# Optimization experiments

Hardware: AMD Instinct MI355X
Metric: run time of the kernel (lower is better)

The kernel has to match this reference:

```python
import jax, jax.numpy as jnp
import numpy as np

# Hyper-params from init_kwargs
H, DM, DA, DP, M, T = 8, 512, 256, 128, 32, 4096
DK, DAh, DPh = DM // H, DA // H, DP // H   # 64, 32, 16
B, K_STEPS = 8, 2048
S = T + K_STEPS          # length of x = memory + x_pre
EPS = 1e-12

def _l2n(x):
    # F.normalize(p=2, dim=-1)
    return x / jnp.maximum(jnp.linalg.norm(x, axis=-1, keepdims=True), EPS)

def setup_inputs() -> dict:
    key = jax.random.key(0)
    ks = jax.random.split(key, 28)
    n = lambda i, s, sc=0.05: jax.random.normal(ks[i], s, jnp.float32) * sc
    return {
        "memory": jax.random.normal(ks[0], (B, S - 1, DM), jnp.float32),
        "x_pre":  jax.random.normal(ks[1], (B, 1, DM), jnp.float32),
        "aux":    jax.random.normal(ks[2], (B, S, DA), jnp.float32),
        "pos":    jax.random.normal(ks[3], (B, S, DP), jnp.float32),
        "Wq": n(4, (H, DK, DM)), "bq": n(5, (H, DK)),
        "Wk": n(6, (H, DK, DM)), "bk": n(7, (H, DK)),
        "Wv": n(8, (H, DK, DM)), "bv": n(9, (H, DK)),
        "Wqa": n(10, (H, DAh, DA)), "bqa": n(11, (H, DAh)),
        "Wka": n(12, (H, DAh, DA)), "bka": n(13, (H, DAh)),
        "Wqp": n(14, (H, DPh, DP)), "bqp": n(15, (H, DPh)),
        "Wkp": n(16, (H, DPh, DP)), "bkp": n(17, (H, DPh)),
        "W_ih": n(18, (3 * DK, DM)), "W_hh": n(19, (3 * DK, DK)),
        "b_ih": n(20, (3 * DK,)), "b_hh": n(21, (3 * DK,)),
        "WO": n(22, (DM, DM)), "bO": n(23, (DM,)),
        "w": n(24, (1, 1), 1.0), "w_a": n(25, (1, 1), 1.0), "w_p": n(26, (1, 1), 1.0),
        "G": (jax.random.uniform(ks[27], (DK, DK)) < 0.5).astype(jnp.int32),
        "k": K_STEPS,
    }

def _forward(memory, x_pre, aux, pos, Wq, bq, Wk, bk, Wv, bv, Wqa, bqa, Wka, bka,
             Wqp, bqp, Wkp, bkp, W_ih, W_hh, b_ih, b_hh, WO, bO, w, w_a, w_p, G, k):
    b = memory.shape[0]
    x = jnp.concatenate([memory, x_pre], axis=1)           # [B, S, DM]
    s = x.shape[1]
    Wn = k + T - M + 1                                     # attention window length
    g = G.astype(x.dtype)
    mask_h = jnp.tile(g, (1, H))[None]                     # [1, DK, DM] per-head SparseLinear mask

    # per-head Q/K node projections (SparseLinear), L2-normalized
    Q = _l2n(jnp.einsum('bsd,hkd->bhsk', x, Wq * mask_h) + bq[None, :, None, :])
    K = _l2n(jnp.einsum('bsd,hkd->bhsk', x, Wk * mask_h) + bk[None, :, None, :])

    # tn_transform_pre: for each position p, mean over the M-step window of Qv[m].K[p+m]
    Qv = Q[:, :, -M:, :]                                   # [B,H,M,DK]
    D = jnp.einsum('bhmd,bhsd->bhms', Qv, K)               # [B,H,M,S]
    p_idx = jnp.arange(Wn)[None, :] + jnp.arange(M)[:, None]   # [M,Wn]
    band = D[:, :, jnp.arange(M)[:, None], p_idx]          # [B,H,M,Wn] band-diagonal gather
    tn = band.mean(axis=2)                                 # [B,H,Wn]

    # aux / pos similarities: only the last query row survives the slice in the source
    QA = _l2n(jnp.einsum('bsa,hca->bhsc', aux, Wqa) + bqa[None, :, None, :])
    KA = _l2n(jnp.einsum('bsa,hca->bhsc', aux, Wka) + bka[None, :, None, :])
    dot2 = jnp.einsum('bhc,bhsc->bhs', QA[:, :, -1, :], KA[:, :, aux.shape[1] - Wn:, :])
    QP = _l2n(jnp.einsum('bsp,hcp->bhsc', pos, Wqp) + bqp[None, :, None, :])
    KP = _l2n(jnp.einsum('bsp,hcp->bhsc', pos, Wkp) + bkp[None, :, None, :])
    dot3 = jnp.einsum('bhc,bhsc->bhs', QP[:, :, -1, :], KP[:, :, pos.shape[1] - Wn:, :])

    attn = jax.nn.softmax(w[0, 0] * tn + w_a[0, 0] * dot2 + w_p[0, 0] * dot3, axis=-1)  # [B,H,Wn]

    # value projection over the history window, weighted by attn[..., :-1]
    xv = x[:, s - Wn:s - 1, :]                             # [B, Wn-1, DM]
    V = jnp.einsum('bsd,hkd->bhsk', xv, Wv * mask_h) + bv[None, :, None, :]
    hist = jnp.einsum('bhw,bhwd->bhd', attn[:, :, :-1], V) # [B,H,DK]

    # sequential GRU over the recent M-1 steps (shared across heads)
    recent = jnp.swapaxes(x[:, -M:-1, :], 0, 1)            # [M-1, B, DM]
    def cell(hprev, xt):
        gi = xt @ W_ih.T + b_ih
        gh = hprev @ W_hh.T + b_hh
        ir, iz, inn = jnp.split(gi, 3, axis=-1)
        hr, hz, hn = jnp.split(gh, 3, axis=-1)
        r = jax.nn.sigmoid(ir + hr)
        z = jax.nn.sigmoid(iz + hz)
        nst = jnp.tanh(inn + r * hn)
        return (1.0 - z) * nst + z * hprev, None
    res, _ = jax.lax.scan(cell, jnp.zeros((b, DK), x.dtype), recent)  # [B, DK]

    # concat per-head deltas (deta[:, :, 1:] just drops the initial zeros column)
    deta = (hist + attn[:, :, -1:] * res[:, None, :]).reshape(b, H * DK)   # [B, DM]
    mask_o = jnp.tile(g, (H, H))                           # [DM, DM] for W_O
    out = x_pre + (deta @ (WO * mask_o).T + bO)[:, None, :]
    return out

def reference(memory, x_pre, aux, pos, Wq, bq, Wk, bk, Wv, bv, Wqa, bqa, Wka, bka,
              Wqp, bqp, Wkp, bkp, W_ih, W_hh, b_ih, b_hh, WO, bO, w, w_a, w_p, G, k):
    return _forward(memory, x_pre, aux, pos, Wq, bq, Wk, bk, Wv, bv, Wqa, bqa, Wka,
                    bka, Wqp, bqp, Wkp, bkp, W_ih, W_hh, b_ih, b_hh, WO, bO,
                    w, w_a, w_p, G, k)
```

## Files before the change

### kernel.cpp

```cpp
#include <hip/hip_runtime.h>
#include <math.h>

#define BB   8
#define S    6144
#define SM1  6143
#define DM   512
#define H    8
#define DK   64
#define M    32
#define WN   6113
#define DA   256
#define DAh  32
#define DP   128
#define DPh  16
#define EPSN 1e-12f

#define WS_WKT    0
#define WS_WKAT   262144
#define WS_WKPT   327680
#define WS_QHAT   344064
#define WS_QAHAT  475136
#define WS_QPHAT  477184
#define WS_LOGITS 478208
#define WS_XBAR   869440
#define WS_ALAST  902208
#define WS_RES    902272
#define WS_GI     902784
#define WS_WQM    950400
#define WS_XBF    1212544
#define N_LOGITS  391232
#define N_XBAR    32768

typedef __attribute__((ext_vector_type(8))) short short8;
typedef __attribute__((ext_vector_type(4))) float f32x4;

__device__ inline unsigned short f2bf(float f) {
    union { float f; unsigned u; } v; v.f = f;
    unsigned r = v.u + 0x7fffu + ((v.u >> 16) & 1u);
    return (unsigned short)(r >> 16);
}
__device__ inline float bf2f(unsigned short u) {
    union { unsigned u; float f; } v; v.u = ((unsigned)u) << 16; return v.f;
}

union S8U { short8 v; unsigned short e[8]; };

#define PREP_NB 2368
#define GI_NB   248
#define XCAST_NB 12288

__global__ __launch_bounds__(256) void prelude_k(
    const float* __restrict__ Wk, const float* __restrict__ Wka,
    const float* __restrict__ Wkp, const float* __restrict__ Wq,
    const int* __restrict__ G,
    unsigned short* __restrict__ wkb, unsigned short* __restrict__ wkab,
    unsigned short* __restrict__ wkpb, float* __restrict__ wqm,
    const float* __restrict__ memory, const float* __restrict__ x_pre,
    const float* __restrict__ W_ih, const float* __restrict__ b_ih,
    float* __restrict__ gi_all, unsigned short* __restrict__ xbf)
{
    int bx = blockIdx.x, tid = threadIdx.x;

    if (bx < PREP_NB) {
        int idx = bx * 256 + tid;
        if (idx < H*DM*DK) {
            int k = idx & 63; int d = (idx >> 6) & 511; int h = idx >> 15;
            float v = Wk[(size_t)(h*DK + k)*DM + d] * (float)G[k*DK + (d & 63)];
            wkb[(size_t)h*DM*DK + (((d >> 3)*DK + k) << 3) + (d & 7)] = f2bf(v);
        }
        int i2 = idx - H*DM*DK;
        if (i2 >= 0 && i2 < H*DA*DAh) {
            int h = i2 >> 13; int r = i2 & 8191;
            int j = r & 7; int f = r >> 3;
            int c = f & 31; int a = (f >> 5)*8 + j;
            wkab[i2] = f2bf(Wka[(size_t)(h*DAh + c)*DA + a]);
        }
        int i3 = idx - H*DM*DK - H*DA*DAh;
        if (i3 >= 0 && i3 < H*DP*DPh) {
            int h = i3 >> 11; int r = i3 & 2047;
            int j = r & 7; int f = r >> 3;
            int c = f & 15; int p = (f >> 4)*8 + j;
            wkpb[i3] = f2bf(Wkp[(size_t)(h*DPh + c)*DP + p]);
        }
        int i4 = idx - H*DM*DK - H*DA*DAh - H*DP*DPh;
        if (i4 >= 0 && i4 < H*DK*DM) {
            int d = i4 & 511; int k = (i4 >> 9) & 63;
            wqm[i4] = Wq[i4] * (float)G[k*DK + (d & 63)];
        }
        return;
    }
    if (bx < PREP_NB + GI_NB) {
        if (tid < 192) {
            int gx = bx - PREP_NB;
            int t = gx >> 3, b = gx & 7, c = tid;
            const float* xr = memory + ((size_t)b*SM1 + (S - M) + t)*DM;
            const float* wr = W_ih + (size_t)c*DM;
            float s = b_ih[c];
            for (int d = 0; d < DM; d += 4) {
                float4 x4 = *(const float4*)(xr + d);
                float4 w4 = *(const float4*)(wr + d);
                s += x4.x*w4.x + x4.y*w4.y + x4.z*w4.z + x4.w*w4.w;
            }
            gi_all[((size_t)t*BB + b)*192 + c] = s;
        }
        return;
    }
    {
        size_t e = ((size_t)(bx - PREP_NB - GI_NB)*256 + tid)*8;
        int b = (int)(e / ((size_t)S*DM));
        size_t r = e - (size_t)b*S*DM;
        int t = (int)(r >> 9);
        int d = (int)(r & 511);
        const float* src = (t < SM1) ? memory + ((size_t)b*SM1 + t)*DM + d
                                     : x_pre + (size_t)b*DM + d;
        float4 v0 = *(const float4*)src, v1 = *(const float4*)(src + 4);
        S8U t8;
        t8.e[0]=f2bf(v0.x); t8.e[1]=f2bf(v0.y); t8.e[2]=f2bf(v0.z); t8.e[3]=f2bf(v0.w);
        t8.e[4]=f2bf(v1.x); t8.e[5]=f2bf(v1.y); t8.e[6]=f2bf(v1.z); t8.e[7]=f2bf(v1.w);
        *(short8*)(xbf + e) = t8.v;
    }
}

__global__ __launch_bounds__(256) void qhat_k2(
    const float* __restrict__ memory, const float* __restrict__ x_pre,
    const float* __restrict__ wqm, const float* __restrict__ bq,
    float* __restrict__ qhat)
{
    int bx = blockIdx.x;
    int mp = bx & 15;
    int h  = (bx >> 4) & 7;
    int b  = bx >> 7;
    int tid = threadIdx.x;
    int k = tid & 63, dq = tid >> 6;

    int m0 = mp*2;
    int t0 = S - M + m0, t1 = t0 + 1;
    const float* x0 = ((t0 < SM1) ? memory + ((size_t)b*SM1 + t0)*DM
                                  : x_pre + (size_t)b*DM) + dq*128;
    const float* x1 = ((t1 < SM1) ? memory + ((size_t)b*SM1 + t1)*DM
                                  : x_pre + (size_t)b*DM) + dq*128;
    const float* wr = wqm + (size_t)(h*DK + k)*DM + dq*128;

    float s0 = 0.f, s1 = 0.f;
    #pragma unroll 8
    for (int d = 0; d < 128; d += 4) {
        float4 w4 = *(const float4*)(wr + d);
        float4 a4 = *(const float4*)(x0 + d);
        float4 b4 = *(const float4*)(x1 + d);
        s0 += w4.x*a4.x + w4.y*a4.y + w4.z*a4.z + w4.w*a4.w;
        s1 += w4.x*b4.x + w4.y*b4.y + w4.z*b4.z + w4.w*b4.w;
    }

    __shared__ float part[2][4][64];
    part[0][dq][k] = s0;
    part[1][dq][k] = s1;
    __syncthreads();

    if (tid < 128) {
        int mi = tid >> 6;
        int kk = tid & 63;
        float q = part[mi][0][kk] + part[mi][1][kk] + part[mi][2][kk] + part[mi][3][kk]
                + bq[h*DK + kk];
        float ss = q*q;
        #pragma unroll
        for (int d2 = 1; d2 <= 32; d2 <<= 1) ss += __shfl_xor(ss, d2);
        qhat[((size_t)(b*H + h)*M + (m0 + mi))*DK + kk] = q / fmaxf(sqrtf(ss), EPSN);
    }
}

__global__ __launch_bounds__(256) void qaqp_k(
    const float* __restrict__ aux, const float* __restrict__ pos,
    const float* __restrict__ Wqa, const float* __restrict__ bqa,
    const float* __restrict__ Wqp, const float* __restrict__ bqp,
    float* __restrict__ qahat, float* __restrict__ qphat)
{
    int bh = blockIdx.x; int b = bh >> 3, h = bh & 7;
    int tid = threadIdx.x;
    __shared__ float pa[32][8];
    __shared__ float pp[16][16];

    {
        int c = tid & 31, ch = tid >> 5;
        const float* ar = aux + ((size_t)b*S + (S-1))*DA + ch*32;
        const float* wv = Wqa + (size_t)(h*DAh + c)*DA + ch*32;
        float s = 0.f;
        #pragma unroll
        for (int a = 0; a < 32; a += 4) {
            float4 a4 = *(const float4*)(ar + a);
            float4 w4 = *(const float4*)(wv + a);
            s += a4.x*w4.x + a4.y*w4.y + a4.z*w4.z + a4.w*w4.w;
        }
        pa[c][ch] = s;
    }
    {
        int c = tid & 15, ch = tid >> 4;
        const float* pr = pos + ((size_t)b*S + (S-1))*DP + ch*8;
        const float* wv = Wqp + (size_t)(h*DPh + c)*DP + ch*8;
        float4 a4 = *(const float4*)(pr);
        float4 w4 = *(const float4*)(wv);
        float4 a5 = *(const float4*)(pr + 4);
        float4 w5 = *(const float4*)(wv + 4);
        pp[c][ch] = a4.x*w4.x + a4.y*w4.y + a4.z*w4.z + a4.w*w4.w
                  + a5.x*w5.x + a5.y*w5.y + a5.z*w5.z + a5.w*w5.w;
    }
    __syncthreads();

    if (tid < 32) {
        float q = bqa[h*DAh + tid];
        #pragma unroll
        for (int ch = 0; ch < 8; ++ch) q += pa[tid][ch];
        float ss = q*q;
        #pragma unroll
        for (int d2 = 1; d2 <= 16; d2 <<= 1) ss += __shfl_xor(ss, d2);
        qahat[(size_t)bh*DAh + tid] = q / fmaxf(sqrtf(ss), EPSN);
    } else if (tid >= 64 && tid < 80) {
        int c = tid - 64;
        float q = bqp[h*DPh + c];
        #pragma unroll
        for (int ch = 0; ch < 16; ++ch) q += pp[c][ch];
        float ss = q*q;
        #pragma unroll
        for (int d2 = 1; d2 <= 8; d2 <<= 1) ss += __shfl_xor(ss, d2);
        qphat[(size_t)bh*DPh + c] = q / fmaxf(sqrtf(ss), EPSN);
    }
}

#define SMEM_BYTES 33280

__device__ __forceinline__ void kproj3_body(int bxx, int tid, unsigned char* smemraw,
    const unsigned short* __restrict__ xbf, const unsigned short* __restrict__ wkb,
    const float* __restrict__ bk, const float* __restrict__ qhat,
    const float* __restrict__ wscal, float* __restrict__ logits)
{
    int tile = bxx % 96, h = (bxx / 96) & 7, b = bxx / (96*8);
    int t0 = tile * 64;
    int wave = tid >> 6, lane = tid & 63;
    int quad = lane >> 4, l16 = lane & 15;

    typedef unsigned short row72[72];
    row72* Qs = (row72*)smemraw;
    row72* Kb = (row72*)(smemraw + 32*72*2);
    float* tnloc = (float*)(smemraw + 96*72*2);

    {
        const float* qsrc = qhat + (size_t)(b*H + h)*M*DK;
        int i = tid * 8;
        float4 a0 = *(const float4*)(qsrc + i);
        float4 a1 = *(const float4*)(qsrc + i + 4);
        S8U t8;
        t8.e[0]=f2bf(a0.x); t8.e[1]=f2bf(a0.y); t8.e[2]=f2bf(a0.z); t8.e[3]=f2bf(a0.w);
        t8.e[4]=f2bf(a1.x); t8.e[5]=f2bf(a1.y); t8.e[6]=f2bf(a1.z); t8.e[7]=f2bf(a1.w);
        *(short8*)&Qs[i >> 6][i & 63] = t8.v;
    }
    if (tid < 95) tnloc[tid] = 0.f;

    f32x4 acc[4];
    #pragma unroll
    for (int nt = 0; nt < 4; ++nt) acc[nt] = (f32x4){0.f,0.f,0.f,0.f};

    const unsigned short* xrow = xbf + ((size_t)b*S + t0 + wave*16 + l16)*DM;
    const unsigned short* wh = wkb + (size_t)h*DM*DK;

    #pragma unroll
    for (int ch = 0; ch < 4; ++ch) {
        #pragma unroll
        for (int ks = 0; ks < 4; ++ks) {
            short8 a = *(const short8*)(xrow + ch*128 + ks*32 + quad*8);
            #pragma unroll
            for (int nt = 0; nt < 4; ++nt) {
                short8 bf = *(const short8*)(wh + (((ch*16 + ks*4 + quad)*DK) + nt*16 + l16)*8);
                acc[nt] = __builtin_amdgcn_mfma_f32_16x16x32_bf16(a, bf, acc[nt], 0, 0, 0);
            }
        }
    }

    {
        float vv[4][4];
        float ss[4] = {0.f, 0.f, 0.f, 0.f};
        #pragma unroll
        for (int nt = 0; nt < 4; ++nt) {
            float bkv = bk[h*DK + nt*16 + l16];
            #pragma unroll
            for (int reg = 0; reg < 4; ++reg) {
                float v = acc[nt][reg] + bkv;
                vv[nt][reg] = v;
                ss[reg] += v*v;
            }
        }
        #pragma unroll
        for (int d2 = 1; d2 <= 8; d2 <<= 1)
            #pragma unroll
            for (int reg = 0; reg < 4; ++reg) ss[reg] += __shfl_xor(ss[reg], d2);
        #pragma unroll
        for (int reg = 0; reg < 4; ++reg) {
            float inv = 1.f / fmaxf(sqrtf(ss[reg]), EPSN);
            #pragma unroll
            for (int nt = 0; nt < 4; ++nt)
                Kb[wave*16 + quad*4 + reg][nt*16 + l16] = f2bf(vv[nt][reg] * inv);
        }
    }
    __syncthreads();

    {
        int mtile = wave & 1;
        int thalf = (wave >> 1) * 32;
        f32x4 acc2[2];
        acc2[0] = (f32x4){0.f,0.f,0.f,0.f};
        acc2[1] = (f32x4){0.f,0.f,0.f,0.f};
        #pragma unroll
        for (int ks = 0; ks < 2; ++ks) {
            short8 a = *(const short8*)&Qs[mtile*16 + l16][ks*32 + quad*8];
            #pragma unroll
            for (int nt = 0; nt < 2; ++nt) {
                short8 kf = *(const short8*)&Kb[thalf + nt*16 + l16][ks*32 + quad*8];
                acc2[nt] = __builtin_amdgcn_mfma_f32_16x16x32_bf16(a, kf, acc2[nt], 0, 0, 0);
            }
        }
        int m0 = mtile*16 + quad*4;
        #pragma unroll
        for (int nt = 0; nt < 2; ++nt) {
            int tl = thalf + nt*16 + l16;
            #pragma unroll
            for (int reg = 0; reg < 4; ++reg) {
                int mm = m0 + reg;
                int j = t0 + tl - mm;
                if (j >= 0 && j < WN)
                    atomicAdd(&tnloc[tl - mm + 31], acc2[nt][reg]);
            }
        }
    }
    __syncthreads();
    if (tid < 95) {
        int j = t0 + tid - 31;
        if (j >= 0 && j < WN)
            atomicAdd(&logits[(size_t)(b*H + h)*WN + j], wscal[0]*(1.f/32.f)*tnloc[tid]);
    }
}

__device__ __forceinline__ void ka_body(int g, int tid, unsigned char* smemraw,
    const float* __restrict__ aux, const unsigned short* __restrict__ wkab,
    const float* __restrict__ bka, const float* __restrict__ qahat,
    const float* __restrict__ wa, float* __restrict__ logits)
{
    int tile = g % 96;
    int b    = g / 96;
    int j0   = tile * 64;
    int wave = tid >> 6, lane = tid & 63;
    int quad = lane >> 4, l16 = lane & 15;

    unsigned short* Xa = (unsigned short*)smemraw;

    {
        int r = tid >> 2, seg = tid & 3;
        int j = j0 + r; if (j > WN-1) j = WN-1;
        const float* ar = aux + ((size_t)b*S + (31 + j))*DA + seg*64;
        int tt = r >> 4, lo = r & 15;
        #pragma unroll
        for (int gg = 0; gg < 8; ++gg) {
            float4 v0 = *(const float4*)(ar + gg*8);
            float4 v1 = *(const float4*)(ar + gg*8 + 4);
            int d0 = seg*64 + gg*8;
            int ks = d0 >> 5, qd = (d0 >> 3) & 3;
            S8U t8;
            t8.e[0]=f2bf(v0.x); t8.e[1]=f2bf(v0.y); t8.e[2]=f2bf(v0.z); t8.e[3]=f2bf(v0.w);
            t8.e[4]=f2bf(v1.x); t8.e[5]=f2bf(v1.y); t8.e[6]=f2bf(v1.z); t8.e[7]=f2bf(v1.w);
            *(short8*)&Xa[(tt*8 + ks)*520 + (qd*16 + lo)*8] = t8.v;
        }
    }
    __syncthreads();

    float wav = wa[0];
    for (int h = 0; h < H; ++h) {
        const unsigned short* wsrc = wkab + (size_t)h*DA*DAh;
        f32x4 acc[2];
        acc[0] = (f32x4){0.f,0.f,0.f,0.f};
        acc[1] = (f32x4){0.f,0.f,0.f,0.f};
        #pragma unroll
        for (int ks = 0; ks < 8; ++ks) {
            short8 a = *(const short8*)&Xa[(wave*8 + ks)*520 + lane*8];
            #pragma unroll
            for (int nt = 0; nt < 2; ++nt) {
                short8 bf = *(const short8*)(wsrc + (size_t)(((ks*4 + quad)*32) + nt*16 + l16)*8);
                acc[nt] = __builtin_amdgcn_mfma_f32_16x16x32_bf16(a, bf, acc[nt], 0, 0, 0);
            }
        }
        float bk0 = bka[h*DAh + l16], bk1 = bka[h*DAh + 16 + l16];
        float q0 = qahat[(size_t)(b*H + h)*DAh + l16];
        float q1 = qahat[(size_t)(b*H + h)*DAh + 16 + l16];
        #pragma unroll
        for (int reg = 0; reg < 4; ++reg) {
            float v0 = acc[0][reg] + bk0;
            float v1 = acc[1][reg] + bk1;
            float ss = v0*v0 + v1*v1;
            float dp = v0*q0 + v1*q1;
            #pragma unroll
            for (int d2 = 1; d2 <= 8; d2 <<= 1) {
                ss += __shfl_xor(ss, d2);
                dp += __shfl_xor(dp, d2);
            }
            if (l16 == 0) {
                int j = j0 + wave*16 + quad*4 + reg;
                if (j < WN)
                    atomicAdd(&logits[(size_t)(b*H + h)*WN + j],
                              wav * dp / fmaxf(sqrtf(ss), EPSN));
            }
        }
    }
}

__device__ __forceinline__ void kp_body(int g, int tid, unsigned char* smemraw,
    const float* __restrict__ pos, const unsigned short* __restrict__ wkpb,
    const float* __restrict__ bkp, const float* __restrict__ qphat,
    const float* __restrict__ wp, float* __restrict__ logits)
{
    int tile = g % 96;
    int b    = g / 96;
    int j0   = tile * 64;
    int wave = tid >> 6, lane = tid & 63;
    int quad = lane >> 4, l16 = lane & 15;

    unsigned short* Xp = (unsigned short*)smemraw;

    {
        int r = tid >> 2, seg = tid & 3;
        int j = j0 + r; if (j > WN-1) j = WN-1;
        const float* pr = pos + ((size_t)b*S + (31 + j))*DP + seg*32;
        int tt = r >> 4, lo = r & 15;
        #pragma unroll
        for (int gg = 0; gg < 4; ++gg) {
            float4 v0 = *(const float4*)(pr + gg*8);
            float4 v1 = *(const float4*)(pr + gg*8 + 4);
            int d0 = seg*32 + gg*8;
            int ks = d0 >> 5, qd = (d0 >> 3) & 3;
            S8U t8;
            t8.e[0]=f2bf(v0.x); t8.e[1]=f2bf(v0.y); t8.e[2]=f2bf(v0.z); t8.e[3]=f2bf(v0.w);
            t8.e[4]=f2bf(v1.x); t8.e[5]=f2bf(v1.y); t8.e[6]=f2bf(v1.z); t8.e[7]=f2bf(v1.w);
            *(short8*)&Xp[(tt*4 + ks)*520 + (qd*16 + lo)*8] = t8.v;
        }
    }
    __syncthreads();

    float wpv = wp[0];
    for (int h = 0; h < H; ++h) {
        const unsigned short* wsrc = wkpb + (size_t)h*DP*DPh;
        f32x4 acc = (f32x4){0.f,0.f,0.f,0.f};
        #pragma unroll
        for (int ks = 0; ks < 4; ++ks) {
            short8 a = *(const short8*)&Xp[(wave*4 + ks)*520 + lane*8];
            short8 bf = *(const short8*)(wsrc + (size_t)(((ks*4 + quad)*16) + l16)*8);
            acc = __builtin_amdgcn_mfma_f32_16x16x32_bf16(a, bf, acc, 0, 0, 0);
        }
        float bk0 = bkp[h*DPh + l16];
        float q0 = qphat[(size_t)(b*H + h)*DPh + l16];
        #pragma unroll
        for (int reg = 0; reg < 4; ++reg) {
            float v = acc[reg] + bk0;
            float ss = v*v;
            float dp = v*q0;
            #pragma unroll
            for (int d2 = 1; d2 <= 8; d2 <<= 1) {
                ss += __shfl_xor(ss, d2);
                dp += __shfl_xor(dp, d2);
            }
            if (l16 == 0) {
                int j = j0 + wave*16 + quad*4 + reg;
                if (j < WN)
                    atomicAdd(&logits[(size_t)(b*H + h)*WN + j],
                              wpv * dp / fmaxf(sqrtf(ss), EPSN));
            }
        }
    }
}

__global__ __launch_bounds__(256, 4) void proj_fused_k(
    const unsigned short* __restrict__ xbf, const unsigned short* __restrict__ wkb,
    const float* __restrict__ bk, const float* __restrict__ qhat,
    const float* __restrict__ w,
    const float* __restrict__ aux, const unsigned short* __restrict__ wkab,
    const float* __restrict__ bka, const float* __restrict__ qahat,
    const float* __restrict__ wa,
    const float* __restrict__ pos, const unsigned short* __restrict__ wkpb,
    const float* __restrict__ bkp, const float* __restrict__ qphat,
    const float* __restrict__ wp,
    float* __restrict__ logits)
{
    __shared__ __align__(16) unsigned char smemraw[SMEM_BYTES];
    int bx = blockIdx.x;
    int g = bx / 10, r = bx - g*10;
    int tid = threadIdx.x;
    if (r < 8)
        kproj3_body(g*8 + r, tid, smemraw, xbf, wkb, bk, qhat, w, logits);
    else if (r == 8)
        ka_body(g, tid, smemraw, aux, wkab, bka, qahat, wa, logits);
    else
        kp_body(g, tid, smemraw, pos, wkpb, bkp, qphat, wp, logits);
}

__global__ __launch_bounds__(256, 2) void ka_only_k(
    const float* __restrict__ aux, const unsigned short* __restrict__ wkab,
    const float* __restrict__ bka, const float* __restrict__ qahat,
    const float* __restrict__ wa, float* __restrict__ logits)
{
    __shared__ __align__(16) unsigned char smemraw[SMEM_BYTES];
    ka_body(blockIdx.x, threadIdx.x, smemraw, aux, wkab, bka, qahat, wa, logits);
}
__global__ __launch_bounds__(256, 2) void kp_only_k(
    const float* __restrict__ pos, const unsigned short* __restrict__ wkpb,
    const float* __restrict__ bkp, const float* __restrict__ qphat,
    const float* __restrict__ wp, float* __restrict__ logits)
{
    __shared__ __align__(16) unsigned char smemraw[SMEM_BYTES];
    kp_body(blockIdx.x, threadIdx.x, smemraw, pos, wkpb, bkp, qphat, wp, logits);
}

__global__ __launch_bounds__(256, 2) void kproj_band_mfma2(
    const float* __restrict__ memory, const float* __restrict__ x_pre,
    const unsigned short* __restrict__ wkb, const float* __restrict__ bk,
    const float* __restrict__ qhat, const float* __restrict__ wscal,
    float* __restrict__ logits)
{
    int bx = blockIdx.x;
    int hp = bx & 3, b = (bx >> 2) & 7, tile = bx >> 5;
    int t0 = tile * 128;
    int tid = threadIdx.x;
    int wave = tid >> 6, lane = tid & 63;
    int quad = lane >> 4, l16 = lane & 15;

    __shared__ unsigned short Xf[32*520];
    __shared__ unsigned short Wf[16*520];
    __shared__ unsigned short Kb[128][72];
    __shared__ unsigned short Qs[M][72];
    __shared__ float tnloc[159];

    if (tid < 159) tnloc[tid] = 0.f;
    {
        int h = hp*2;
        const float* qsrc = qhat + (size_t)(b*H + h)*M*DK;
        int i = tid * 8;
        float4 a0 = *(const float4*)(qsrc + i);
        float4 a1 = *(const float4*)(qsrc + i + 4);
        S8U t8;
        t8.e[0]=f2bf(a0.x); t8.e[1]=f2bf(a0.y); t8.e[2]=f2bf(a0.z); t8.e[3]=f2bf(a0.w);
        t8.e[4]=f2bf(a1.x); t8.e[5]=f2bf(a1.y); t8.e[6]=f2bf(a1.z); t8.e[7]=f2bf(a1.w);
        *(short8*)&Qs[i >> 6][i & 63] = t8.v;
    }

    f32x4 acc[2][2][4];
    #pragma unroll
    for (int hi = 0; hi < 2; ++hi)
        #pragma unroll
        for (int mt = 0; mt < 2; ++mt)
            #pragma unroll
            for (int nt = 0; nt < 4; ++nt) acc[hi][mt][nt] = (f32x4){0.f,0.f,0.f,0.f};

    for (int ch = 0; ch < 4; ++ch) {
        __syncthreads();
        {
            int r = tid >> 1, half = tid & 1;
            int t = t0 + r;
            const float* xr = ((t < SM1) ? (memory + ((size_t)b*SM1 + t)*DM)
                                         : (x_pre + (size_t)b*DM)) + ch*128 + half*64;
            int tt = r >> 4, lo = r & 15;
            #pragma unroll
            for (int g = 0; g < 8; ++g) {
                float4 v0 = *(const float4*)(xr + g*8);
                float4 v1 = *(const float4*)(xr + g*8 + 4);
                int d0 = half*64 + g*8;
                int ks = d0 >> 5, qd = (d0 >> 3) & 3;
                S8U t8;
                t8.e[0]=f2bf(v0.x); t8.e[1]=f2bf(v0.y); t8.e[2]=f2bf(v0.z); t8.e[3]=f2bf(v0.w);
                t8.e[4]=f2bf(v1.x); t8.e[5]=f2bf(v1.y); t8.e[6]=f2bf(v1.z); t8.e[7]=f2bf(v1.w);
                *(short8*)&Xf[(tt*4 + ks)*520 + (qd*16 + lo)*8] = t8.v;
            }
        }
        {
// ... 160 lines not shown
    }
    float inv = 1.f / red[0];
    for (int j = tid; j < WN; j += 1024) {
        float a = expf(L[j] - mx) * inv;
        L[j] = a;
        if (j == WN-1) alast[bh] = a;
    }
}

#define JC2 96
__global__ __launch_bounds__(256) void xbar_bf_k(
    const unsigned short* __restrict__ xbf, const float* __restrict__ attn,
    float* __restrict__ xbar)
{
    int chunk = blockIdx.x & 63;
    int b = blockIdx.x >> 6;
    int j0 = chunk * JC2;
    int lim = (WN-1) - j0; if (lim > JC2) lim = JC2; if (lim < 0) lim = 0;
    __shared__ float al[H][JC2];
    int tid = threadIdx.x;
    for (int i = tid; i < H*JC2; i += 256) {
        int hh = i / JC2, jj = i - hh*JC2;
        al[hh][jj] = (jj < lim) ? attn[(size_t)(b*H + hh)*WN + j0 + jj] : 0.f;
    }
    __syncthreads();
    int d0 = tid * 2;
    const unsigned* p = (const unsigned*)(xbf + ((size_t)b*S + 31 + j0)*DM + d0);
    float acc[H][2];
    #pragma unroll
    for (int hh = 0; hh < H; ++hh) { acc[hh][0] = 0.f; acc[hh][1] = 0.f; }
    #pragma unroll 4
    for (int jj = 0; jj < lim; ++jj) {
        unsigned u = p[(size_t)jj*(DM/2)];
        float x0 = bf2f((unsigned short)(u & 0xffff));
        float x1 = bf2f((unsigned short)(u >> 16));
        #pragma unroll
        for (int hh = 0; hh < H; ++hh) {
            float a = al[hh][jj];
            acc[hh][0] += a * x0;
            acc[hh][1] += a * x1;
        }
    }
    #pragma unroll
    for (int hh = 0; hh < H; ++hh) {
        atomicAdd(&xbar[(size_t)(b*H+hh)*DM + d0],     acc[hh][0]);
        atomicAdd(&xbar[(size_t)(b*H+hh)*DM + d0 + 1], acc[hh][1]);
    }
}

#define JC 191
__global__ __launch_bounds__(256) void xbar_k(
    const float* __restrict__ memory, const float* __restrict__ attn,
    float* __restrict__ xbar)
{
    int chunk = blockIdx.x & 31;
    int b = blockIdx.x >> 5;
    int j0 = chunk * JC;
    __shared__ float al[H][JC];
    int tid = threadIdx.x;
    for (int i = tid; i < H*JC; i += 256) {
        int hh = i / JC, jj = i - hh*JC;
        al[hh][jj] = attn[(size_t)(b*H + hh)*WN + j0 + jj];
    }
    __syncthreads();
    int d0 = tid * 2;
    float acc[H][2];
    #pragma unroll
    for (int hh = 0; hh < H; ++hh) { acc[hh][0] = 0.f; acc[hh][1] = 0.f; }
    for (int jj = 0; jj < JC; ++jj) {
        int t = 31 + j0 + jj;
        const float2 xv = *(const float2*)(memory + ((size_t)b*SM1 + t)*DM + d0);
        #pragma unroll
        for (int hh = 0; hh < H; ++hh) {
            float a = al[hh][jj];
            acc[hh][0] += a * xv.x;
            acc[hh][1] += a * xv.y;
        }
    }
    #pragma unroll
    for (int hh = 0; hh < H; ++hh) {
        atomicAdd(&xbar[(size_t)(b*H+hh)*DM + d0],     acc[hh][0]);
        atomicAdd(&xbar[(size_t)(b*H+hh)*DM + d0 + 1], acc[hh][1]);
    }
}

__global__ __launch_bounds__(512) void gru_scan(
    const float* __restrict__ gi_all, const float* __restrict__ W_hh,
    const float* __restrict__ b_hh, float* __restrict__ res)
{
    int b = threadIdx.x >> 6;
    int l = threadIdx.x & 63;

    float w0[64], w1[64], w2[64];
    {
        const float* r0p = W_hh + (size_t)l*DK;
        const float* r1p = W_hh + (size_t)(64 + l)*DK;
        const float* r2p = W_hh + (size_t)(128 + l)*DK;
        #pragma unroll
        for (int i = 0; i < 16; ++i) {
            float4 a = *(const float4*)(r0p + i*4);
            w0[i*4]=a.x; w0[i*4+1]=a.y; w0[i*4+2]=a.z; w0[i*4+3]=a.w;
            float4 c = *(const float4*)(r1p + i*4);
            w1[i*4]=c.x; w1[i*4+1]=c.y; w1[i*4+2]=c.z; w1[i*4+3]=c.w;
            float4 e = *(const float4*)(r2p + i*4);
            w2[i*4]=e.x; w2[i*4+1]=e.y; w2[i*4+2]=e.z; w2[i*4+3]=e.w;
        }
    }
    float bh0 = b_hh[l], bh1 = b_hh[64 + l], bh2 = b_hh[128 + l];

    float h = 0.f;
    const float* g0 = gi_all + (size_t)b*192;
    float gr = g0[l], gz = g0[64 + l], gn = g0[128 + l];

    #pragma unroll 1
    for (int t = 0; t < 31; ++t) {
        float a0 = bh0, a1 = bh1, a2 = bh2;
        #pragma unroll
        for (int k = 0; k < 64; ++k) {
            float hk = __int_as_float(__builtin_amdgcn_readlane(__float_as_int(h), k));
            a0 += hk * w0[k];
            a1 += hk * w1[k];
            a2 += hk * w2[k];
        }
        float ngr = 0.f, ngz = 0.f, ngn = 0.f;
        if (t < 30) {
            const float* g2 = gi_all + ((size_t)(t+1)*BB + b)*192;
            ngr = g2[l]; ngz = g2[64 + l]; ngn = g2[128 + l];
        }
        float r = 1.f / (1.f + expf(-(gr + a0)));
        float z = 1.f / (1.f + expf(-(gz + a1)));
        float n = tanhf(gn + r * a2);
        h = (1.f - z)*n + z*h;
        gr = ngr; gz = ngz; gn = ngn;
    }
    res[b*DK + l] = h;
}

__global__ __launch_bounds__(512) void final_k(
    const float* __restrict__ x_pre, const float* __restrict__ xbar,
    const float* __restrict__ Wv, const float* __restrict__ bv,
    const float* __restrict__ WO, const float* __restrict__ bO,
    const float* __restrict__ alast, const float* __restrict__ res,
    const int* __restrict__ G, float* __restrict__ out)
{
    int b = blockIdx.x;
    int tid = threadIdx.x;
    __shared__ float gl[64*64];
    __shared__ float deta[512];
    for (int i = tid; i < 4096; i += 512) gl[i] = (float)G[(i & 63)*64 + (i >> 6)];
    __syncthreads();
    int h = tid >> 6, dk = tid & 63;
    float ala = alast[b*H + h];
    const float* xb  = xbar + (size_t)(b*H + h)*DM;
    const float* wvr = Wv + (size_t)tid*DM;
    const float* gcol = gl + dk;
    float s = 0.f;
    for (int e = 0; e < DM; e += 4) {
        float4 wv4 = *(const float4*)(wvr + e);
        float4 xb4 = *(const float4*)(xb + e);
        int eb = e & 63;
        s += wv4.x*gcol[eb*64]     *xb4.x + wv4.y*gcol[(eb+1)*64]*xb4.y
           + wv4.z*gcol[(eb+2)*64]*xb4.z + wv4.w*gcol[(eb+3)*64]*xb4.w;
    }
    float hist = s + bv[tid]*(1.f - ala);
    deta[tid] = hist + ala * res[b*DK + dk];
    __syncthreads();
    int dpos = tid;
    const float* wor = WO + (size_t)dpos*DM;
    const float* gcol2 = gl + (dpos & 63);
    float o = 0.f;
    for (int jj = 0; jj < DM; jj += 4) {
        float4 wo4 = *(const float4*)(wor + jj);
        int jb = jj & 63;
        o += wo4.x*gcol2[jb*64]     *deta[jj]   + wo4.y*gcol2[(jb+1)*64]*deta[jj+1]
           + wo4.z*gcol2[(jb+2)*64]*deta[jj+2] + wo4.w*gcol2[(jb+3)*64]*deta[jj+3];
    }
    out[(size_t)b*DM + dpos] = x_pre[(size_t)b*DM + dpos] + o + bO[dpos];
}

extern "C" void kernel_launch(void* const* d_in, const int* in_sizes, int n_in,
                              void* d_out, int out_size, void* d_ws, size_t ws_size,
                              hipStream_t stream)
{
    const float* memory = (const float*)d_in[0];
    const float* x_pre  = (const float*)d_in[1];
    const float* aux    = (const float*)d_in[2];
    const float* pos    = (const float*)d_in[3];
    const float* Wq  = (const float*)d_in[4];
    const float* bq  = (const float*)d_in[5];
    const float* Wk  = (const float*)d_in[6];
    const float* bk  = (const float*)d_in[7];
    const float* Wv  = (const float*)d_in[8];
    const float* bv  = (const float*)d_in[9];
    const float* Wqa = (const float*)d_in[10];
    const float* bqa = (const float*)d_in[11];
    const float* Wka = (const float*)d_in[12];
    const float* bka = (const float*)d_in[13];
    const float* Wqp = (const float*)d_in[14];
    const float* bqp = (const float*)d_in[15];
    const float* Wkp = (const float*)d_in[16];
    const float* bkp = (const float*)d_in[17];
    const float* W_ih = (const float*)d_in[18];
    const float* W_hh = (const float*)d_in[19];
    const float* b_ih = (const float*)d_in[20];
    const float* b_hh = (const float*)d_in[21];
    const float* WO  = (const float*)d_in[22];
    const float* bO  = (const float*)d_in[23];
    const float* w   = (const float*)d_in[24];
    const float* w_a = (const float*)d_in[25];
    const float* w_p = (const float*)d_in[26];
    const int*   G   = (const int*)d_in[27];
    (void)in_sizes; (void)n_in; (void)out_size;

    float* ws = (float*)d_ws;
    unsigned short* wkb  = (unsigned short*)(ws + WS_WKT);
    unsigned short* wkab = (unsigned short*)(ws + WS_WKAT);
    unsigned short* wkpb = (unsigned short*)(ws + WS_WKPT);
    float* qhat   = ws + WS_QHAT;
    float* qahat  = ws + WS_QAHAT;
    float* qphat  = ws + WS_QPHAT;
    float* logits = ws + WS_LOGITS;
    float* xbar   = ws + WS_XBAR;
    float* alast  = ws + WS_ALAST;
    float* resb   = ws + WS_RES;
    float* gi_all = ws + WS_GI;
    float* wqm    = ws + WS_WQM;
    unsigned short* xbf = (unsigned short*)(ws + WS_XBF);
    float* outp   = (float*)d_out;

    const size_t need = ((size_t)WS_XBF + 12582912) * 4;
    const bool big = (ws_size >= need);

    hipMemsetAsync(logits, 0, (size_t)(N_LOGITS + N_XBAR)*sizeof(float), stream);

    prelude_k<<<big ? (PREP_NB + GI_NB + XCAST_NB) : (PREP_NB + GI_NB), 256, 0, stream>>>(
        Wk, Wka, Wkp, Wq, G, wkb, wkab, wkpb, wqm,
        memory, x_pre, W_ih, b_ih, gi_all, xbf);

    qhat_k2<<<BB*H*16, 256, 0, stream>>>(memory, x_pre, wqm, bq, qhat);
    qaqp_k<<<BB*H, 256, 0, stream>>>(aux, pos, Wqa, bqa, Wqp, bqp, qahat, qphat);
    gru_scan<<<1, 512, 0, stream>>>(gi_all, W_hh, b_hh, resb);

    if (big) {
        proj_fused_k<<<7680, 256, 0, stream>>>(
            xbf, wkb, bk, qhat, w,
            aux, wkab, bka, qahat, w_a,
            pos, wkpb, bkp, qphat, w_p, logits);
    } else {
        kproj_band_mfma2<<<48*BB*4, 256, 0, stream>>>(memory, x_pre, wkb, bk, qhat,
                                                      w, logits);
        ka_only_k<<<BB*96, 256, 0, stream>>>(aux, wkab, bka, qahat, w_a, logits);
        kp_only_k<<<BB*96, 256, 0, stream>>>(pos, wkpb, bkp, qphat, w_p, logits);
    }

    softmax_k<<<BB*H, 1024, 0, stream>>>(logits, alast);

    if (big)
        xbar_bf_k<<<BB*64, 256, 0, stream>>>(xbf, logits, xbar);
    else
        xbar_k<<<BB*32, 256, 0, stream>>>(memory, logits, xbar);

    final_k<<<BB, 512, 0, stream>>>(x_pre, xbar, Wv, bv, WO, bO, alast, resb, G, outp);
}
```

Before: 615.6 us.

## Fuse small launches, stage K-proj activations in LDS, and split aux/pos heads across blocks

Folds the qa/qp query projection into the prelude kernel and merges the qhat and GRU-scan kernels into one launch, so the GRU now runs as two blocks of four batches each. This cuts the number of kernel launches and lets the tiny serial GRU overlap with the qhat blocks. The K-projection body now stages each activation chunk in shared memory through a register prefetch pipeline instead of reading it straight from global memory. The aux/pos logit bodies are split so each block handles two heads instead of eight, and the fused projection grid is regrouped from 10 to 4 slots per group for more parallelism. The costs are extra barriers, more shared memory per block, and the aux/pos tiles being reloaded once per head pair.

```diff
diff --git a/kernel.cpp b/kernel.cpp
--- a/kernel.cpp
+++ b/kernel.cpp
@@ -45,8 +45,9 @@
 
 union S8U { short8 v; unsigned short e[8]; };
 
-#define PREP_NB 2368
-#define GI_NB   248
+#define PREP_NB  2368
+#define GI_NB    248
+#define QAQP_NB  64
 #define XCAST_NB 12288
 
 __global__ __launch_bounds__(256) void prelude_k(
@@ -57,9 +58,15 @@
     unsigned short* __restrict__ wkpb, float* __restrict__ wqm,
     const float* __restrict__ memory, const float* __restrict__ x_pre,
     const float* __restrict__ W_ih, const float* __restrict__ b_ih,
-    float* __restrict__ gi_all, unsigned short* __restrict__ xbf)
+    float* __restrict__ gi_all, unsigned short* __restrict__ xbf,
+    const float* __restrict__ aux, const float* __restrict__ pos,
+    const float* __restrict__ Wqa, const float* __restrict__ bqa,
+    const float* __restrict__ Wqp, const float* __restrict__ bqp,
+    float* __restrict__ qahat, float* __restrict__ qphat)
 {
     int bx = blockIdx.x, tid = threadIdx.x;
+    __shared__ float pa[32][8];
+    __shared__ float pp[16][16];
 
     if (bx < PREP_NB) {
         int idx = bx * 256 + tid;
@@ -105,8 +112,56 @@
         }
         return;
     }
+    if (bx < PREP_NB + GI_NB + QAQP_NB) {
+        int bh = bx - PREP_NB - GI_NB;
+        int b = bh >> 3, h = bh & 7;
+        {
+            int c = tid & 31, ch = tid >> 5;
+            const float* ar = aux + ((size_t)b*S + (S-1))*DA + ch*32;
+            const float* wv = Wqa + (size_t)(h*DAh + c)*DA + ch*32;
+            float s = 0.f;
+            #pragma unroll
+            for (int a = 0; a < 32; a += 4) {
+                float4 a4 = *(const float4*)(ar + a);
+                float4 w4 = *(const float4*)(wv + a);
+                s += a4.x*w4.x + a4.y*w4.y + a4.z*w4.z + a4.w*w4.w;
+            }
+            pa[c][ch] = s;
+        }
+        {
+            int c = tid & 15, ch = tid >> 4;
+            const float* pr = pos + ((size_t)b*S + (S-1))*DP + ch*8;
+            const float* wv = Wqp + (size_t)(h*DPh + c)*DP + ch*8;
+            float4 a4 = *(const float4*)(pr);
+            float4 w4 = *(const float4*)(wv);
+            float4 a5 = *(const float4*)(pr + 4);
+            float4 w5 = *(const float4*)(wv + 4);
+            pp[c][ch] = a4.x*w4.x + a4.y*w4.y + a4.z*w4.z + a4.w*w4.w
+                      + a5.x*w5.x + a5.y*w5.y + a5.z*w5.z + a5.w*w5.w;
+        }
+        __syncthreads();
+        if (tid < 32) {
+            float q = bqa[h*DAh + tid];
+            #pragma unroll
+            for (int ch = 0; ch < 8; ++ch) q += pa[tid][ch];
+            float ss = q*q;
+            #pragma unroll
+            for (int d2 = 1; d2 <= 16; d2 <<= 1) ss += __shfl_xor(ss, d2);
+            qahat[(size_t)bh*DAh + tid] = q / fmaxf(sqrtf(ss), EPSN);
+        } else if (tid >= 64 && tid < 80) {
+            int c = tid - 64;
+            float q = bqp[h*DPh + c];
+            #pragma unroll
+            for (int ch = 0; ch < 16; ++ch) q += pp[c][ch];
+            float ss = q*q;
+            #pragma unroll
+            for (int d2 = 1; d2 <= 8; d2 <<= 1) ss += __shfl_xor(ss, d2);
+            qphat[(size_t)bh*DPh + c] = q / fmaxf(sqrtf(ss), EPSN);
+        }
+        return;
+    }
     {
-        size_t e = ((size_t)(bx - PREP_NB - GI_NB)*256 + tid)*8;
+        size_t e = ((size_t)(bx - PREP_NB - GI_NB - QAQP_NB)*256 + tid)*8;
         int b = (int)(e / ((size_t)S*DM));
         size_t r = e - (size_t)b*S*DM;
         int t = (int)(r >> 9);
@@ -121,107 +176,106 @@
     }
 }
 
-__global__ __launch_bounds__(256) void qhat_k2(
+__global__ __launch_bounds__(256) void qhat_gru_k(
     const float* __restrict__ memory, const float* __restrict__ x_pre,
     const float* __restrict__ wqm, const float* __restrict__ bq,
-    float* __restrict__ qhat)
+    float* __restrict__ qhat,
+    const float* __restrict__ gi_all, const float* __restrict__ W_hh,
+    const float* __restrict__ b_hh, float* __restrict__ res)
 {
     int bx = blockIdx.x;
-    int mp = bx & 15;
-    int h  = (bx >> 4) & 7;
-    int b  = bx >> 7;
     int tid = threadIdx.x;
-    int k = tid & 63, dq = tid >> 6;
-
-    int m0 = mp*2;
-    int t0 = S - M + m0, t1 = t0 + 1;
-    const float* x0 = ((t0 < SM1) ? memory + ((size_t)b*SM1 + t0)*DM
-                                  : x_pre + (size_t)b*DM) + dq*128;
-    const float* x1 = ((t1 < SM1) ? memory + ((size_t)b*SM1 + t1)*DM
-                                  : x_pre + (size_t)b*DM) + dq*128;
-    const float* wr = wqm + (size_t)(h*DK + k)*DM + dq*128;
-
-    float s0 = 0.f, s1 = 0.f;
-    #pragma unroll 8
-    for (int d = 0; d < 128; d += 4) {
-        float4 w4 = *(const float4*)(wr + d);
-        float4 a4 = *(const float4*)(x0 + d);
-        float4 b4 = *(const float4*)(x1 + d);
-        s0 += w4.x*a4.x + w4.y*a4.y + w4.z*a4.z + w4.w*a4.w;
-        s1 += w4.x*b4.x + w4.y*b4.y + w4.z*b4.z + w4.w*b4.w;
-    }
-
     __shared__ float part[2][4][64];
-    part[0][dq][k] = s0;
-    part[1][dq][k] = s1;
-    __syncthreads();
-
-    if (tid < 128) {
-        int mi = tid >> 6;
-        int kk = tid & 63;
-        float q = part[mi][0][kk] + part[mi][1][kk] + part[mi][2][kk] + part[mi][3][kk]
-                + bq[h*DK + kk];
-        float ss = q*q;
-        #pragma unroll
-        for (int d2 = 1; d2 <= 32; d2 <<= 1) ss += __shfl_xor(ss, d2);
-        qhat[((size_t)(b*H + h)*M + (m0 + mi))*DK + kk] = q / fmaxf(sqrtf(ss), EPSN);
-    }
-}
-
-__global__ __launch_bounds__(256) void qaqp_k(
-    const float* __restrict__ aux, const float* __restrict__ pos,
-    const float* __restrict__ Wqa, const float* __restrict__ bqa,
-    const float* __restrict__ Wqp, const float* __restrict__ bqp,
-    float* __restrict__ qahat, float* __restrict__ qphat)
-{
-    int bh = blockIdx.x; int b = bh >> 3, h = bh & 7;
-    int tid = threadIdx.x;
-    __shared__ float pa[32][8];
-    __shared__ float pp[16][16];
+
+    if (bx < 1024) {
+        int mp = bx & 15;
+        int h  = (bx >> 4) & 7;
+        int b  = bx >> 7;
+        int k = tid & 63, dq = tid >> 6;
+
+        int m0 = mp*2;
+        int t0 = S - M + m0, t1 = t0 + 1;
+        const float* x0 = ((t0 < SM1) ? memory + ((size_t)b*SM1 + t0)*DM
+                                      : x_pre + (size_t)b*DM) + dq*128;
+        const float* x1 = ((t1 < SM1) ? memory + ((size_t)b*SM1 + t1)*DM
+                                      : x_pre + (size_t)b*DM) + dq*128;
+        const float* wr = wqm + (size_t)(h*DK + k)*DM + dq*128;
+
+        float s0 = 0.f, s1 = 0.f;
+        #pragma unroll 8
+        for (int d = 0; d < 128; d += 4) {
+            float4 w4 = *(const float4*)(wr + d);
+            float4 a4 = *(const float4*)(x0 + d);
+            float4 b4 = *(const float4*)(x1 + d);
+            s0 += w4.x*a4.x + w4.y*a4.y + w4.z*a4.z + w4.w*a4.w;
+            s1 += w4.x*b4.x + w4.y*b4.y + w4.z*b4.z + w4.w*b4.w;
+        }
+
+        part[0][dq][k] = s0;
+        part[1][dq][k] = s1;
+        __syncthreads();
+
+        if (tid < 128) {
+            int mi = tid >> 6;
+            int kk = tid & 63;
+            float q = part[mi][0][kk] + part[mi][1][kk] + part[mi][2][kk] + part[mi][3][kk]
+                    + bq[h*DK + kk];
+            float ss = q*q;
+            #pragma unroll
+            for (int d2 = 1; d2 <= 32; d2 <<= 1) ss += __shfl_xor(ss, d2);
+            qhat[((size_t)(b*H + h)*M + (m0 + mi))*DK + kk] = q / fmaxf(sqrtf(ss), EPSN);
+        }
+        return;
+    }
 
     {
-        int c = tid & 31, ch = tid >> 5;
-        const float* ar = aux + ((size_t)b*S + (S-1))*DA + ch*32;
-        const float* wv = Wqa + (size_t)(h*DAh + c)*DA + ch*32;
-        float s = 0.f;
-        #pragma unroll
-        for (int a = 0; a < 32; a += 4) {
-            float4 a4 = *(const float4*)(ar + a);
-            float4 w4 = *(const float4*)(wv + a);
-            s += a4.x*w4.x + a4.y*w4.y + a4.z*w4.z + a4.w*w4.w;
-        }
-        pa[c][ch] = s;
-    }
-    {
-        int c = tid & 15, ch = tid >> 4;
-        const float* pr = pos + ((size_t)b*S + (S-1))*DP + ch*8;
-        const float* wv = Wqp + (size_t)(h*DPh + c)*DP + ch*8;
-        float4 a4 = *(const float4*)(pr);
-        float4 w4 = *(const float4*)(wv);
-        float4 a5 = *(const float4*)(pr + 4);
-        float4 w5 = *(const float4*)(wv + 4);
-        pp[c][ch] = a4.x*w4.x + a4.y*w4.y + a4.z*w4.z + a4.w*w4.w
-                  + a5.x*w5.x + a5.y*w5.y + a5.z*w5.z + a5.w*w5.w;
-    }
-    __syncthreads();
-
-    if (tid < 32) {
-        float q = bqa[h*DAh + tid];
-        #pragma unroll
-        for (int ch = 0; ch < 8; ++ch) q += pa[tid][ch];
-        float ss = q*q;
-        #pragma unroll
-        for (int d2 = 1; d2 <= 16; d2 <<= 1) ss += __shfl_xor(ss, d2);
-        qahat[(size_t)bh*DAh + tid] = q / fmaxf(sqrtf(ss), EPSN);
-    } else if (tid >= 64 && tid < 80) {
-        int c = tid - 64;
-        float q = bqp[h*DPh + c];
-        #pragma unroll
-        for (int ch = 0; ch < 16; ++ch) q += pp[c][ch];
-        float ss = q*q;
-        #pragma unroll
-        for (int d2 = 1; d2 <= 8; d2 <<= 1) ss += __shfl_xor(ss, d2);
-        qphat[(size_t)bh*DPh + c] = q / fmaxf(sqrtf(ss), EPSN);
+        int bg = bx - 1024;
+        int b = bg*4 + (tid >> 6);
+        int l = tid & 63;
+
+        float w0[64], w1[64], w2[64];
+        {
+            const float* r0p = W_hh + (size_t)l*DK;
+            const float* r1p = W_hh + (size_t)(64 + l)*DK;
+            const float* r2p = W_hh + (size_t)(128 + l)*DK;
+            #pragma unroll
+            for (int i = 0; i < 16; ++i) {
+                float4 a = *(const float4*)(r0p + i*4);
+                w0[i*4]=a.x; w0[i*4+1]=a.y; w0[i*4+2]=a.z; w0[i*4+3]=a.w;
+                float4 c = *(const float4*)(r1p + i*4);
+                w1[i*4]=c.x; w1[i*4+1]=c.y; w1[i*4+2]=c.z; w1[i*4+3]=c.w;
+                float4 e = *(const float4*)(r2p + i*4);
+                w2[i*4]=e.x; w2[i*4+1]=e.y; w2[i*4+2]=e.z; w2[i*4+3]=e.w;
+            }
+        }
+        float bh0 = b_hh[l], bh1 = b_hh[64 + l], bh2 = b_hh[128 + l];
+
+        float h = 0.f;
+        const float* g0 = gi_all + (size_t)b*192;
+        float gr = g0[l], gz = g0[64 + l], gn = g0[128 + l];
+
+        #pragma unroll 1
+        for (int t = 0; t < 31; ++t) {
+            float a0 = bh0, a1 = bh1, a2 = bh2;
+            #pragma unroll
+            for (int k = 0; k < 64; ++k) {
+                float hk = __int_as_float(__builtin_amdgcn_readlane(__float_as_int(h), k));
+                a0 += hk * w0[k];
+                a1 += hk * w1[k];
+                a2 += hk * w2[k];
+            }
+            float ngr = 0.f, ngz = 0.f, ngn = 0.f;
+            if (t < 30) {
+                const float* g2 = gi_all + ((size_t)(t+1)*BB + b)*192;
+                ngr = g2[l]; ngz = g2[64 + l]; ngn = g2[128 + l];
+            }
+            float r = 1.f / (1.f + expf(-(gr + a0)));
+            float z = 1.f / (1.f + expf(-(gz + a1)));
+            float n = tanhf(gn + r * a2);
+            h = (1.f - z)*n + z*h;
+            gr = ngr; gz = ngz; gn = ngn;
+        }
+        res[b*DK + l] = h;
     }
 }
 
@@ -237,10 +291,12 @@
     int wave = tid >> 6, lane = tid & 63;
     int quad = lane >> 4, l16 = lane & 15;
 
+    typedef unsigned short row136[136];
     typedef unsigned short row72[72];
-    row72* Qs = (row72*)smemraw;
-    row72* Kb = (row72*)(smemraw + 32*72*2);
-    float* tnloc = (float*)(smemraw + 96*72*2);
+    row136* Axf = (row136*)smemraw;
+    row72*  Qs  = (row72*)(smemraw + 17408);
+    row72*  Kb  = (row72*)(smemraw + 22016);
+    float* tnloc = (float*)(smemraw + 31232);
 
     {
         const float* qsrc = qhat + (size_t)(b*H + h)*M*DK;
@@ -258,14 +314,34 @@
     #pragma unroll
     for (int nt = 0; nt < 4; ++nt) acc[nt] = (f32x4){0.f,0.f,0.f,0.f};
 
-    const unsigned short* xrow = xbf + ((size_t)b*S + t0 + wave*16 + l16)*DM;
     const unsigned short* wh = wkb + (size_t)h*DM*DK;
+
+    int srow = tid >> 2, sseg = tid & 3;
+    const unsigned short* asrc = xbf + ((size_t)b*S + t0 + srow)*DM + sseg*32;
+
+    short8 r0 = *(const short8*)(asrc);
+    short8 r1 = *(const short8*)(asrc + 8);
+    short8 r2 = *(const short8*)(asrc + 16);
+    short8 r3 = *(const short8*)(asrc + 24);
 
     #pragma unroll
     for (int ch = 0; ch < 4; ++ch) {
+        if (ch) __syncthreads();
+        *(short8*)&Axf[srow][sseg*32]      = r0;
+        *(short8*)&Axf[srow][sseg*32 + 8]  = r1;
+        *(short8*)&Axf[srow][sseg*32 + 16] = r2;
+        *(short8*)&Axf[srow][sseg*32 + 24] = r3;
+        __syncthreads();
+        if (ch < 3) {
+            const unsigned short* nsrc = asrc + (ch+1)*128;
+            r0 = *(const short8*)(nsrc);
+            r1 = *(const short8*)(nsrc + 8);
+            r2 = *(const short8*)(nsrc + 16);
+            r3 = *(const short8*)(nsrc + 24);
+        }
         #pragma unroll
         for (int ks = 0; ks < 4; ++ks) {
-            short8 a = *(const short8*)(xrow + ch*128 + ks*32 + quad*8);
+            short8 a = *(const short8*)&Axf[wave*16 + l16][ks*32 + quad*8];
             #pragma unroll
             for (int nt = 0; nt < 4; ++nt) {
                 short8 bf = *(const short8*)(wh + (((ch*16 + ks*4 + quad)*DK) + nt*16 + l16)*8);
@@ -343,7 +419,8 @@
     const float* __restrict__ wa, float* __restrict__ logits)
 {
     int tile = g % 96;
-    int b    = g / 96;
+    int hp   = (g / 96) & 3;
+    int b    = g / 384;
     int j0   = tile * 64;
     int wave = tid >> 6, lane = tid & 63;
     int quad = lane >> 4, l16 = lane & 15;
@@ -370,7 +447,9 @@
     __syncthreads();
 
     float wav = wa[0];
-    for (int h = 0; h < H; ++h) {
+    #pragma unroll
+    for (int hi = 0; hi < 2; ++hi) {
+        int h = hp*2 + hi;
         const unsigned short* wsrc = wkab + (size_t)h*DA*DAh;
         f32x4 acc[2];
         acc[0] = (f32x4){0.f,0.f,0.f,0.f};
@@ -414,7 +493,8 @@
     const float* __restrict__ wp, float* __restrict__ logits)
 {
     int tile = g % 96;
-    int b    = g / 96;
+    int hp   = (g / 96) & 3;
+    int b    = g / 384;
     int j0   = tile * 64;
     int wave = tid >> 6, lane = tid & 63;
     int quad = lane >> 4, l16 = lane & 15;
@@ -441,7 +521,9 @@
     __syncthreads();
 
     float wpv = wp[0];
-    for (int h = 0; h < H; ++h) {
+    #pragma unroll
+    for (int hi = 0; hi < 2; ++hi) {
+        int h = hp*2 + hi;
         const unsigned short* wsrc = wkpb + (size_t)h*DP*DPh;
         f32x4 acc = (f32x4){0.f,0.f,0.f,0.f};
         #pragma unroll
@@ -472,6 +554,7 @@
     }
 }
 
+#define KA_NB 3072
 __global__ __launch_bounds__(256, 4) void proj_fused_k(
     const unsigned short* __restrict__ xbf, const unsigned short* __restrict__ wkb,
     const float* __restrict__ bk, const float* __restrict__ qhat,
@@ -486,11 +569,11 @@
 {
     __shared__ __align__(16) unsigned char smemraw[SMEM_BYTES];
     int bx = blockIdx.x;
-    int g = bx / 10, r = bx - g*10;
+    int g = bx >> 2, r = bx & 3;
     int tid = threadIdx.x;
-    if (r < 8)
-        kproj3_body(g*8 + r, tid, smemraw, xbf, wkb, bk, qhat, w, logits);
-    else if (r == 8)
+    if (r < 2)
+        kproj3_body(g*2 + r, tid, smemraw, xbf, wkb, bk, qhat, w, logits);
+    else if (r == 2)
         ka_body(g, tid, smemraw, aux, wkab, bka, qahat, wa, logits);
     else
         kp_body(g, tid, smemraw, pos, wkpb, bkp, qphat, wp, logits);
@@ -817,58 +900,6 @@
         atomicAdd(&xbar[(size_t)(b*H+hh)*DM + d0],     acc[hh][0]);
         atomicAdd(&xbar[(size_t)(b*H+hh)*DM + d0 + 1], acc[hh][1]);
     }
-}
-
-__global__ __launch_bounds__(512) void gru_scan(
-    const float* __restrict__ gi_all, const float* __restrict__ W_hh,
-    const float* __restrict__ b_hh, float* __restrict__ res)
-{
-    int b = threadIdx.x >> 6;
-    int l = threadIdx.x & 63;
-
-    float w0[64], w1[64], w2[64];
-    {
-        const float* r0p = W_hh + (size_t)l*DK;
-        const float* r1p = W_hh + (size_t)(64 + l)*DK;
-        const float* r2p = W_hh + (size_t)(128 + l)*DK;
-        #pragma unroll
-        for (int i = 0; i < 16; ++i) {
-            float4 a = *(const float4*)(r0p + i*4);
-            w0[i*4]=a.x; w0[i*4+1]=a.y; w0[i*4+2]=a.z; w0[i*4+3]=a.w;
-            float4 c = *(const float4*)(r1p + i*4);
-            w1[i*4]=c.x; w1[i*4+1]=c.y; w1[i*4+2]=c.z; w1[i*4+3]=c.w;
-            float4 e = *(const float4*)(r2p + i*4);
-            w2[i*4]=e.x; w2[i*4+1]=e.y; w2[i*4+2]=e.z; w2[i*4+3]=e.w;
-        }
-    }
-    float bh0 = b_hh[l], bh1 = b_hh[64 + l], bh2 = b_hh[128 + l];
-
-    float h = 0.f;
-    const float* g0 = gi_all + (size_t)b*192;
-    float gr = g0[l], gz = g0[64 + l], gn = g0[128 + l];
-
-    #pragma unroll 1
-    for (int t = 0; t < 31; ++t) {
-        float a0 = bh0, a1 = bh1, a2 = bh2;
-        #pragma unroll
-        for (int k = 0; k < 64; ++k) {
-            float hk = __int_as_float(__builtin_amdgcn_readlane(__float_as_int(h), k));
-            a0 += hk * w0[k];
-            a1 += hk * w1[k];
-            a2 += hk * w2[k];
-        }
-        float ngr = 0.f, ngz = 0.f, ngn = 0.f;
-        if (t < 30) {
-            const float* g2 = gi_all + ((size_t)(t+1)*BB + b)*192;
-            ngr = g2[l]; ngz = g2[64 + l]; ngn = g2[128 + l];
-        }
-        float r = 1.f / (1.f + expf(-(gr + a0)));
-        float z = 1.f / (1.f + expf(-(gz + a1)));
-        float n = tanhf(gn + r * a2);
-        h = (1.f - z)*n + z*h;
-        gr = ngr; gz = ngz; gn = ngn;
-    }
-    res[b*DK + l] = h;
 }
 
 __global__ __launch_bounds__(512) void final_k(
@@ -968,24 +999,25 @@
 
     hipMemsetAsync(logits, 0, (size_t)(N_LOGITS + N_XBAR)*sizeof(float), stream);
 
-    prelude_k<<<big ? (PREP_NB + GI_NB + XCAST_NB) : (PREP_NB + GI_NB), 256, 0, stream>>>(
+    prelude_k<<<big ? (PREP_NB + GI_NB + QAQP_NB + XCAST_NB)
+                    : (PREP_NB + GI_NB + QAQP_NB), 256, 0, stream>>>(
         Wk, Wka, Wkp, Wq, G, wkb, wkab, wkpb, wqm,
-        memory, x_pre, W_ih, b_ih, gi_all, xbf);
-
-    qhat_k2<<<BB*H*16, 256, 0, stream>>>(memory, x_pre, wqm, bq, qhat);
-    qaqp_k<<<BB*H, 256, 0, stream>>>(aux, pos, Wqa, bqa, Wqp, bqp, qahat, qphat);
-    gru_scan<<<1, 512, 0, stream>>>(gi_all, W_hh, b_hh, resb);
+        memory, x_pre, W_ih, b_ih, gi_all, xbf,
+        aux, pos, Wqa, bqa, Wqp, bqp, qahat, qphat);
+
+    qhat_gru_k<<<1026, 256, 0, stream>>>(memory, x_pre, wqm, bq, qhat,
+                                         gi_all, W_hh, b_hh, resb);
 
     if (big) {
-        proj_fused_k<<<7680, 256, 0, stream>>>(
+        proj_fused_k<<<12288, 256, 0, stream>>>(
             xbf, wkb, bk, qhat, w,
             aux, wkab, bka, qahat, w_a,
             pos, wkpb, bkp, qphat, w_p, logits);
     } else {
         kproj_band_mfma2<<<48*BB*4, 256, 0, stream>>>(memory, x_pre, wkb, bk, qhat,
                                                       w, logits);
-        ka_only_k<<<BB*96, 256, 0, stream>>>(aux, wkab, bka, qahat, w_a, logits);
-        kp_only_k<<<BB*96, 256, 0, stream>>>(pos, wkpb, bkp, qphat, w_p, logits);
+        ka_only_k<<<KA_NB, 256, 0, stream>>>(aux, wkab, bka, qahat, w_a, logits);
+        kp_only_k<<<KA_NB, 256, 0, stream>>>(pos, wkpb, bkp, qphat, w_p, logits);
     }
 
     softmax_k<<<BB*H, 1024, 0, stream>>>(logits, alast);
```

Result: slower. 636.9 us (+3.5%).
